# Kernel optimization log

Hardware: AMD Instinct MI355X
Metric: run time of the kernel (lower is better)

## Reference

```python
import jax, jax.numpy as jnp
import numpy as np

N_HEADS = 16
EMBED_DIM = 1024
HEAD_DIM = EMBED_DIM // N_HEADS  # 64
SRC_LEN = 64  # shifted-causal mask: key j visible iff j <= i + SRC_LEN
THETA = 10000.0


def _rope_tables(T, D, dtype):
    # angles[t, p] = t / theta^(2p/D), p in [0, D/2)
    freqs = 1.0 / (THETA ** (jnp.arange(0, D, 2, dtype=jnp.float32) / D))  # [D/2]
    ang = jnp.arange(T, dtype=jnp.float32)[:, None] * freqs[None, :]       # [T, D/2]
    return jnp.cos(ang).astype(dtype), jnp.sin(ang).astype(dtype)


def _apply_rope(x, cos, sin):
    # x: [B, T, H, D]; pairs along last dim act as complex numbers
    B, T, H, D = x.shape
    xp = x.reshape(B, T, H, D // 2, 2)
    x0, x1 = xp[..., 0], xp[..., 1]
    c = cos[None, :, None, :]  # [1, T, 1, D/2]
    s = sin[None, :, None, :]
    o0 = x0 * c - x1 * s
    o1 = x0 * s + x1 * c
    return jnp.stack([o0, o1], axis=-1).reshape(B, T, H, D)


def setup_inputs() -> dict:
    key = jax.random.key(0)
    ks = jax.random.split(key, 9)
    B, T, C = 2, 2048, EMBED_DIM
    sc = 1.0 / np.sqrt(C)
    inp = {
        "x_1": jax.random.normal(ks[0], (B, T, C), dtype=jnp.float32),
        "x_2": jax.random.normal(ks[1], (B, T, C), dtype=jnp.float32),
        "wq": jax.random.normal(ks[2], (C, C), dtype=jnp.float32) * sc,
        "bq": jax.random.normal(ks[3], (C,), dtype=jnp.float32) * sc,
        "wk": jax.random.normal(ks[4], (C, C), dtype=jnp.float32) * sc,
        "bk": jax.random.normal(ks[5], (C,), dtype=jnp.float32) * sc,
        "wv": jax.random.normal(ks[6], (C, C), dtype=jnp.float32) * sc,
        "bv": jax.random.normal(ks[7], (C,), dtype=jnp.float32) * sc,
        "wp": jax.random.normal(ks[8], (C, C), dtype=jnp.float32) * sc,
    }
    return inp


def reference(x_1, x_2, wq, bq, wk, bk, wv, bv, wp):
    B, T, C = x_1.shape
    H, D = N_HEADS, HEAD_DIM
    q = (x_1 @ wq.T + bq).reshape(B, T, H, D)
    k = (x_2 @ wk.T + bk).reshape(B, T, H, D)
    v = (x_2 @ wv.T + bv).reshape(B, T, H, D)
    cos, sin = _rope_tables(T, D, x_1.dtype)
    q = _apply_rope(q, cos, sin)
    k = _apply_rope(k, cos, sin)
    # attention with shifted causal mask
    attn = jnp.einsum("bihd,bjhd->bhij", q, k) * (D ** -0.5)
    i = jnp.arange(T)
    mask = i[None, :] <= i[:, None] + SRC_LEN  # [T, T], True = visible
    attn = jnp.where(mask[None, None, :, :], attn, -jnp.inf)
    attn = jax.nn.softmax(attn, axis=-1)
    out = jnp.einsum("bhij,bjhd->bihd", attn, v).reshape(B, T, C)
    return out @ wp.T
```

## Files before the change

kernel.cpp:

```cpp
#include <hip/hip_runtime.h>
#include <hip/hip_bf16.h>

typedef __bf16 v8bf __attribute__((ext_vector_type(8)));
typedef float  v4f  __attribute__((ext_vector_type(4)));

#define T_LEN 2048
#define NH 16
#define HD 64
#define BH 32
#define C_DIM 1024
#define SCQ 0.1803368801111737f

#define WS_X1B  ((size_t)0)
#define WS_X2B  ((size_t)8  << 20)
#define WS_W    ((size_t)16 << 20)
#define WS_CTAB ((size_t)24 << 20)
#define WS_STAB (WS_CTAB + 262144)
#define WS_Q    ((size_t)25 << 20)
#define WS_K    ((size_t)33 << 20)
#define WS_VT   ((size_t)41 << 20)
#define WS_O    ((size_t)0)

__device__ __forceinline__ unsigned short f2bf(float f) {
  unsigned int u = __float_as_uint(f);
  u += 0x7fffu + ((u >> 16) & 1u);
  return (unsigned short)(u >> 16);
}
__device__ __forceinline__ float bf2f(unsigned short h) {
  return __uint_as_float(((unsigned int)h) << 16);
}

__device__ __forceinline__ float xg_sum(float m) {
  m = m + __shfl_xor(m, 16, 64);
  m = m + __shfl_xor(m, 32, 64);
  return m;
}
__device__ __forceinline__ unsigned int packbf2hw(float lo, float hi) {
  unsigned short a = __builtin_bit_cast(unsigned short, (__bf16)lo);
  unsigned short b = __builtin_bit_cast(unsigned short, (__bf16)hi);
  return (unsigned int)a | ((unsigned int)b << 16);
}

__global__ __launch_bounds__(256) void cvt_kernel(
    const float* __restrict__ x1, const float* __restrict__ x2,
    const float* __restrict__ wq, const float* __restrict__ wk,
    const float* __restrict__ wv, const float* __restrict__ wp,
    unsigned short* __restrict__ x1b, unsigned short* __restrict__ x2b,
    unsigned short* __restrict__ wqb) {
  int i = blockIdx.x * 256 + threadIdx.x;
  if (i >= 3145728) return;
  const float* s; unsigned short* d; int off;
  if (i < 1048576) { s = x1; d = x1b; off = i; }
  else if (i < 2097152) { s = x2; d = x2b; off = i - 1048576; }
  else {
    int j = i - 2097152;
    int w = j >> 18;
    off = j & 262143;
    s = (w == 0) ? wq : (w == 1) ? wk : (w == 2) ? wv : wp;
    d = wqb + ((size_t)w * 1048576);
  }
  float4 v = ((const float4*)s)[off];
  ushort4 o;
  o.x = f2bf(v.x); o.y = f2bf(v.y); o.z = f2bf(v.z); o.w = f2bf(v.w);
  ((ushort4*)d)[off] = o;
}

__global__ __launch_bounds__(256) void tab_kernel(float* __restrict__ ctab,
                                                  float* __restrict__ stab) {
  int i = blockIdx.x * 256 + threadIdx.x;
  int t = i >> 5, f = i & 31;
  float freq = powf(10000.0f, -(float)f * (1.0f / 32.0f));
  float a = (float)t * freq;
  ctab[i] = cosf(a);
  stab[i] = sinf(a);
}

__global__ __launch_bounds__(256) void qk_gemm(
    const unsigned short* __restrict__ x1b, const unsigned short* __restrict__ x2b,
    const unsigned short* __restrict__ wall,
    const float* __restrict__ bq, const float* __restrict__ bk,
    const float* __restrict__ ctab, const float* __restrict__ stab,
    unsigned short* __restrict__ Qd, unsigned short* __restrict__ Kd) {
  int z = blockIdx.z;
  const unsigned short* A = (z == 0) ? x1b : x2b;
  const unsigned short* W = wall + (size_t)z * 1048576;
  const float* bias = (z == 0) ? bq : bk;
  unsigned short* dst = (z == 0) ? Qd : Kd;
  float scale = (z == 0) ? SCQ : 1.0f;

  __shared__ unsigned short lds[2][8192];
  int tid = threadIdx.x;
  int wave = tid >> 6, lane = tid & 63;
  int wm = wave >> 1, wn = wave & 1;
  int r = lane & 15, g = lane >> 4;
  int phys = blockIdx.y * (int)gridDim.x + blockIdx.x;
  int logical = (phys & 7) * 32 + (phys >> 3);
  int m0 = (logical >> 3) * 128, n0 = (logical & 7) * 128;
  int s3 = r & 3;

  v4f zero = {0.f, 0.f, 0.f, 0.f};
  v4f acc[4][4];
#pragma unroll
  for (int i = 0; i < 4; ++i)
#pragma unroll
    for (int j = 0; j < 4; ++j) acc[i][j] = zero;

  auto stage = [&](int b, int k0) {
    const unsigned short* Ab = A + (size_t)m0 * 1024 + k0;
    const unsigned short* Bb = W + (size_t)n0 * 1024 + k0;
#pragma unroll
    for (int it = 0; it < 2; ++it) {
      int c = it * 256 + tid;
      int row = c >> 2;
      int sc = (c & 3) ^ (row & 3);
      __builtin_amdgcn_global_load_lds(
          (const __attribute__((address_space(1))) void*)(Ab + (size_t)row * 1024 + sc * 8),
          (__attribute__((address_space(3))) void*)(&lds[b][0] + it * 2048 + wave * 512),
          16, 0, 0);
      __builtin_amdgcn_global_load_lds(
          (const __attribute__((address_space(1))) void*)(Bb + (size_t)row * 1024 + sc * 8),
          (__attribute__((address_space(3))) void*)(&lds[b][4096] + it * 2048 + wave * 512),
          16, 0, 0);
    }
  };

  stage(0, 0);
  asm volatile("s_waitcnt vmcnt(0)");
  __syncthreads();
  int cur = 0;

  for (int k0 = 0; k0 < 1024; k0 += 32) {
    if (k0 + 32 < 1024) stage(cur ^ 1, k0 + 32);
    v8bf af[4], bfr[4];
#pragma unroll
    for (int mf = 0; mf < 4; ++mf)
      af[mf] = *(const v8bf*)(&lds[cur][0] + (wm * 64 + mf * 16 + r) * 32 + ((g ^ s3) << 3));
#pragma unroll
    for (int nf = 0; nf < 4; ++nf)
      bfr[nf] = *(const v8bf*)(&lds[cur][4096] + (wn * 64 + nf * 16 + r) * 32 + ((g ^ s3) << 3));
#pragma unroll
    for (int mf = 0; mf < 4; ++mf)
#pragma unroll
      for (int nf = 0; nf < 4; ++nf)
        acc[mf][nf] = __builtin_amdgcn_mfma_f32_16x16x32_bf16(bfr[nf], af[mf], acc[mf][nf], 0, 0, 0);
    asm volatile("s_waitcnt vmcnt(0)");
    __syncthreads();
    cur ^= 1;
  }

#pragma unroll
  for (int mf = 0; mf < 4; ++mf) {
    int t = m0 + wm * 64 + mf * 16 + r;
    int b = t >> 11, tt = t & 2047;
#pragma unroll
    for (int nf = 0; nf < 4; ++nf) {
      int c0 = n0 + wn * 64 + nf * 16 + g * 4;
      int h = c0 >> 6, dh = c0 & 63;
      float4 b4 = *(const float4*)(bias + c0);
      int f0 = (dh >> 1);
      float2 cp = *(const float2*)(ctab + tt * 32 + f0);
      float2 sp = *(const float2*)(stab + tt * 32 + f0);
      float x0 = acc[mf][nf][0] + b4.x, x1 = acc[mf][nf][1] + b4.y;
      float x2 = acc[mf][nf][2] + b4.z, x3 = acc[mf][nf][3] + b4.w;
      ushort4 pk;
      pk.x = f2bf((x0 * cp.x - x1 * sp.x) * scale);
      pk.y = f2bf((x0 * sp.x + x1 * cp.x) * scale);
      pk.z = f2bf((x2 * cp.y - x3 * sp.y) * scale);
      pk.w = f2bf((x2 * sp.y + x3 * cp.y) * scale);
      *(ushort4*)(dst + (((size_t)(b * NH + h)) * T_LEN + tt) * HD + dh) = pk;
    }
  }
}

__global__ __launch_bounds__(256) void v_gemm(
    const unsigned short* __restrict__ x2b, const unsigned short* __restrict__ wv,
    const float* __restrict__ bv, unsigned short* __restrict__ VTd) {
  __shared__ unsigned short lds[2][8192];
  int tid = threadIdx.x;
  int wave = tid >> 6, lane = tid & 63;
  int wm = wave >> 1, wn = wave & 1;
  int r = lane & 15, g = lane >> 4;
  int phys = blockIdx.y * (int)gridDim.x + blockIdx.x;
  int logical = (phys & 7) * 32 + (phys >> 3);
  int m0 = (logical >> 3) * 128, n0 = (logical & 7) * 128;
  int s3 = r & 3;

  v4f zero = {0.f, 0.f, 0.f, 0.f};
  v4f acc[4][4];
#pragma unroll
  for (int i = 0; i < 4; ++i)
#pragma unroll
    for (int j = 0; j < 4; ++j) acc[i][j] = zero;

  auto stage = [&](int b, int k0) {
    const unsigned short* Ab = x2b + (size_t)m0 * 1024 + k0;
    const unsigned short* Bb = wv + (size_t)n0 * 1024 + k0;
#pragma unroll
    for (int it = 0; it < 2; ++it) {
      int c = it * 256 + tid;
      int row = c >> 2;
      int sc = (c & 3) ^ (row & 3);
      __builtin_amdgcn_global_load_lds(
          (const __attribute__((address_space(1))) void*)(Ab + (size_t)row * 1024 + sc * 8),
          (__attribute__((address_space(3))) void*)(&lds[b][0] + it * 2048 + wave * 512),
          16, 0, 0);
      __builtin_amdgcn_global_load_lds(
          (const __attribute__((address_space(1))) void*)(Bb + (size_t)row * 1024 + sc * 8),
          (__attribute__((address_space(3))) void*)(&lds[b][4096] + it * 2048 + wave * 512),
          16, 0, 0);
    }
  };

  stage(0, 0);
  asm volatile("s_waitcnt vmcnt(0)");
  __syncthreads();
  int cur = 0;

  for (int k0 = 0; k0 < 1024; k0 += 32) {
    if (k0 + 32 < 1024) stage(cur ^ 1, k0 + 32);
    v8bf af[4], bfr[4];
#pragma unroll
    for (int mf = 0; mf < 4; ++mf)
      af[mf] = *(const v8bf*)(&lds[cur][0] + (wm * 64 + mf * 16 + r) * 32 + ((g ^ s3) << 3));
#pragma unroll
    for (int nf = 0; nf < 4; ++nf)
      bfr[nf] = *(const v8bf*)(&lds[cur][4096] + (wn * 64 + nf * 16 + r) * 32 + ((g ^ s3) << 3));
#pragma unroll
    for (int mf = 0; mf < 4; ++mf)
#pragma unroll
      for (int nf = 0; nf < 4; ++nf)
        acc[mf][nf] = __builtin_amdgcn_mfma_f32_16x16x32_bf16(af[mf], bfr[nf], acc[mf][nf], 0, 0, 0);
    asm volatile("s_waitcnt vmcnt(0)");
    __syncthreads();
    cur ^= 1;
  }
#pragma unroll
  for (int nf = 0; nf < 4; ++nf) {
    int col = n0 + wn * 64 + nf * 16 + r;
    float bv_ = bv[col];
    int h = col >> 6, d = col & 63;
#pragma unroll
    for (int mf = 0; mf < 4; ++mf) {
      int row0 = m0 + wm * 64 + mf * 16 + g * 4;
      int b = row0 >> 11, t0 = row0 & 2047;
      ushort4 pk;
      pk.x = f2bf(acc[mf][nf][0] + bv_);
      pk.y = f2bf(acc[mf][nf][1] + bv_);
      pk.z = f2bf(acc[mf][nf][2] + bv_);
      pk.w = f2bf(acc[mf][nf][3] + bv_);
      *(ushort4*)(VTd + (((size_t)(b * NH + h)) * HD + d) * T_LEN + t0) = pk;
    }
  }
}

__global__ __launch_bounds__(256, 2) void attn_kernel(
    const unsigned short* __restrict__ Qd, const unsigned short* __restrict__ Kd,
    const unsigned short* __restrict__ VTd, unsigned short* __restrict__ Od) {
  int bh = blockIdx.x;
  int qt = (int)gridDim.y - 1 - (int)blockIdx.y;
  int tid = threadIdx.x, wave = tid >> 6, lane = tid & 63;
  int r = lane & 15, g = lane >> 4;
  int qmin = qt * 64 + wave * 16;
  const unsigned short* Qp = Qd + (size_t)bh * T_LEN * HD;
  const unsigned short* Kp = Kd + (size_t)bh * T_LEN * HD;
  const unsigned short* Vp = VTd + (size_t)bh * HD * T_LEN;

  __shared__ unsigned short kv[2][2][4096];
  __shared__ unsigned short plds[4][1024];

  v8bf qf0 = *(const v8bf*)(Qp + (size_t)(qmin + r) * HD + g * 8);
  v8bf qf1 = *(const v8bf*)(Qp + (size_t)(qmin + r) * HD + 32 + g * 8);

  v4f zero = {0.f, 0.f, 0.f, 0.f};
  v4f minus8 = {-8.f, -8.f, -8.f, -8.f};
  v4f oacc[4];
#pragma unroll
  for (int dt = 0; dt < 4; ++dt) oacc[dt] = zero;
  float li = 0.f;

  int ktiles = qt + 2; if (ktiles > 32) ktiles = 32;

  auto stage = [&](int b, int kt) {
    int j0 = kt * 64;
    const unsigned short* Kt = Kp + (size_t)j0 * HD;
#pragma unroll
    for (int is = 0; is < 2; ++is) {
      int q = is * 256 + tid;
      int row = q >> 3, c = q & 7;
      int swc = (c ^ (row & 7)) << 3;
      __builtin_amdgcn_global_load_lds(
          (const __attribute__((address_space(1))) void*)(Kt + row * 64 + swc),
          (__attribute__((address_space(3))) void*)(&kv[b][0][0] + is * 2048 + wave * 512),
          16, 0, 0);
      __builtin_amdgcn_global_load_lds(
          (const __attribute__((address_space(1))) void*)(Vp + (size_t)row * T_LEN + j0 + swc),
          (__attribute__((address_space(3))) void*)(&kv[b][1][0] + is * 2048 + wave * 512),
          16, 0, 0);
    }
  };

  stage(0, 0);
  asm volatile("s_waitcnt vmcnt(0)");
  __syncthreads();
  int cur = 0;

  unsigned short* plw = &plds[wave][0];
  int s7 = r & 7;
  int s8 = s7 << 3;

  for (int kt = 0; kt < ktiles; ++kt) {
    if (kt + 1 < ktiles) stage(cur ^ 1, kt + 1);
    int j0 = kt * 64;
    const unsigned short* kb = &kv[cur][0][0];
    const unsigned short* vb = &kv[cur][1][0];
    v8bf kf0[4], kf1[4], vf0[4], vf1[4];
#pragma unroll
    for (int nt = 0; nt < 4; ++nt) {
      int row = (nt * 16 + r) * 64;
      kf0[nt] = *(const v8bf*)(kb + row + ((g ^ s7) << 3));
      kf1[nt] = *(const v8bf*)(kb + row + (((4 + g) ^ s7) << 3));
      vf0[nt] = *(const v8bf*)(vb + row + ((g ^ s7) << 3));
      vf1[nt] = *(const v8bf*)(vb + row + (((4 + g) ^ s7) << 3));
    }
    v4f s[4];
#pragma unroll
    for (int nt = 0; nt < 4; ++nt) {
      v4f a = minus8;
      a = __builtin_amdgcn_mfma_f32_16x16x32_bf16(kf0[nt], qf0, a, 0, 0, 0);
      a = __builtin_amdgcn_mfma_f32_16x16x32_bf16(kf1[nt], qf1, a, 0, 0, 0);
      s[nt] = a;
    }
    if (j0 + 63 > qmin + 64) {
      int qi64 = qmin + r + 64;
#pragma unroll
      for (int nt = 0; nt < 4; ++nt)
#pragma unroll
        for (int rg = 0; rg < 4; ++rg) {
          int kj = j0 + nt * 16 + g * 4 + rg;
          if (kj > qi64) s[nt][rg] = -1e30f;
        }
    }
    float rs = 0.f;
#pragma unroll
    for (int nt = 0; nt < 4; ++nt)
#pragma unroll
      for (int rg = 0; rg < 4; ++rg) {
        float p = exp2f(s[nt][rg]);
        s[nt][rg] = p;
        rs += p;
      }
    li += rs;
#pragma unroll
    for (int nt = 0; nt < 4; ++nt) {
      uint2 w2;
      w2.x = packbf2hw(s[nt][0], s[nt][1]);
      w2.y = packbf2hw(s[nt][2], s[nt][3]);
      *(uint2*)(plw + r * 64 + (((nt << 4) + (g << 2)) ^ s8)) = w2;
    }
    v8bf pb0 = *(const v8bf*)(plw + r * 64 + ((g ^ s7) << 3));
    v8bf pb1 = *(const v8bf*)(plw + r * 64 + (((4 + g) ^ s7) << 3));
#pragma unroll
    for (int dt = 0; dt < 4; ++dt) {
      oacc[dt] = __builtin_amdgcn_mfma_f32_16x16x32_bf16(vf0[dt], pb0, oacc[dt], 0, 0, 0);
      oacc[dt] = __builtin_amdgcn_mfma_f32_16x16x32_bf16(vf1[dt], pb1, oacc[dt], 0, 0, 0);
    }
    asm volatile("s_waitcnt vmcnt(0)");
    __syncthreads();
    cur ^= 1;
  }
  float rli = 1.0f / xg_sum(li);
#pragma unroll
  for (int dt = 0; dt < 4; ++dt) {
    ushort4 pk;
    pk.x = __builtin_bit_cast(unsigned short, (__bf16)(oacc[dt][0] * rli));
    pk.y = __builtin_bit_cast(unsigned short, (__bf16)(oacc[dt][1] * rli));
    pk.z = __builtin_bit_cast(unsigned short, (__bf16)(oacc[dt][2] * rli));
    pk.w = __builtin_bit_cast(unsigned short, (__bf16)(oacc[dt][3] * rli));
    *(ushort4*)(Od + ((size_t)bh * T_LEN + qmin + r) * HD + dt * 16 + g * 4) = pk;
  }
}

__global__ __launch_bounds__(256) void proj_gemm(
    const unsigned short* __restrict__ Ob, const unsigned short* __restrict__ Wpb,
    float* __restrict__ out) {
  __shared__ unsigned short lds[2][8192];
  int tid = threadIdx.x;
  int wave = tid >> 6, lane = tid & 63;
  int wm = wave >> 1, wn = wave & 1;
  int r = lane & 15, g = lane >> 4;
  int phys = blockIdx.y * (int)gridDim.x + blockIdx.x;
  int logical = (phys & 7) * 32 + (phys >> 3);
  int m0 = (logical >> 3) * 128, n0 = (logical & 7) * 128;
  int s3 = r & 3;

  v4f zero = {0.f, 0.f, 0.f, 0.f};
  v4f acc[4][4];
#pragma unroll
  for (int i = 0; i < 4; ++i)
#pragma unroll
    for (int j = 0; j < 4; ++j) acc[i][j] = zero;

  auto stage = [&](int b, int k0) {
    int h = k0 >> 6;
#pragma unroll
    for (int it = 0; it < 2; ++it) {
      int c = it * 256 + tid;
      int row = c >> 2;
      int sc = (c & 3) ^ (row & 3);
      int k = k0 + sc * 8;
      int d = k & 63;
      int mrow = m0 + row;
      int bb = mrow >> 11, t = mrow & 2047;
      __builtin_amdgcn_global_load_lds(
          (const __attribute__((address_space(1))) void*)(Ob + (((size_t)(bb * NH + h)) * T_LEN + t) * HD + d),
          (__attribute__((address_space(3))) void*)(&lds[b][0] + it * 2048 + wave * 512),
          16, 0, 0);
      __builtin_amdgcn_global_load_lds(
          (const __attribute__((address_space(1))) void*)(Wpb + (size_t)(n0 + row) * 1024 + k),
          (__attribute__((address_space(3))) void*)(&lds[b][4096] + it * 2048 + wave * 512),
          16, 0, 0);
    }
  };

  stage(0, 0);
  asm volatile("s_waitcnt vmcnt(0)");
  __syncthreads();
  int cur = 0;

  for (int k0 = 0; k0 < 1024; k0 += 32) {
    if (k0 + 32 < 1024) stage(cur ^ 1, k0 + 32);
    v8bf af[4], bfr[4];
#pragma unroll
    for (int mf = 0; mf < 4; ++mf)
      af[mf] = *(const v8bf*)(&lds[cur][0] + (wm * 64 + mf * 16 + r) * 32 + ((g ^ s3) << 3));
#pragma unroll
    for (int nf = 0; nf < 4; ++nf)
      bfr[nf] = *(const v8bf*)(&lds[cur][4096] + (wn * 64 + nf * 16 + r) * 32 + ((g ^ s3) << 3));
#pragma unroll
    for (int mf = 0; mf < 4; ++mf)
#pragma unroll
      for (int nf = 0; nf < 4; ++nf)
        acc[mf][nf] = __builtin_amdgcn_mfma_f32_16x16x32_bf16(af[mf], bfr[nf], acc[mf][nf], 0, 0, 0);
    asm volatile("s_waitcnt vmcnt(0)");
    __syncthreads();
    cur ^= 1;
  }
#pragma unroll
  for (int mf = 0; mf < 4; ++mf)
#pragma unroll
    for (int nf = 0; nf < 4; ++nf) {
      int col = n0 + wn * 64 + nf * 16 + r;
      int row0 = m0 + wm * 64 + mf * 16 + g * 4;
#pragma unroll
      for (int rg = 0; rg < 4; ++rg)
        out[(size_t)(row0 + rg) * 1024 + col] = acc[mf][nf][rg];
    }
}

extern "C" void kernel_launch(void* const* d_in, const int* in_sizes, int n_in,
                              void* d_out, int out_size, void* d_ws, size_t ws_size,
                              hipStream_t stream) {
  const float* x1 = (const float*)d_in[0];
  const float* x2 = (const float*)d_in[1];
  const float* wq = (const float*)d_in[2];
  const float* bq = (const float*)d_in[3];
  const float* wk = (const float*)d_in[4];
  const float* bk = (const float*)d_in[5];
  const float* wv = (const float*)d_in[6];
  const float* bv = (const float*)d_in[7];
  const float* wp = (const float*)d_in[8];
  float* out = (float*)d_out;
  char* ws = (char*)d_ws;

  unsigned short* x1b = (unsigned short*)(ws + WS_X1B);
  unsigned short* x2b = (unsigned short*)(ws + WS_X2B);
  unsigned short* wqb = (unsigned short*)(ws + WS_W);
  unsigned short* wvb = wqb + 2 * 1048576;
  unsigned short* wpb = wqb + 3 * 1048576;
  float* ctab = (float*)(ws + WS_CTAB);
  float* stab = (float*)(ws + WS_STAB);
  unsigned short* Qd = (unsigned short*)(ws + WS_Q);
  unsigned short* Kd = (unsigned short*)(ws + WS_K);
  unsigned short* VTd = (unsigned short*)(ws + WS_VT);
  unsigned short* Od = (unsigned short*)(ws + WS_O);

  cvt_kernel<<<12288, 256, 0, stream>>>(x1, x2, wq, wk, wv, wp, x1b, x2b, wqb);
  tab_kernel<<<256, 256, 0, stream>>>(ctab, stab);
  qk_gemm<<<dim3(8, 32, 2), 256, 0, stream>>>(x1b, x2b, wqb, bq, bk, ctab, stab, Qd, Kd);
  v_gemm<<<dim3(8, 32), 256, 0, stream>>>(x2b, wvb, bv, VTd);
  attn_kernel<<<dim3(32, 32), 256, 0, stream>>>(Qd, Kd, VTd, Od);
  proj_gemm<<<dim3(8, 32), 256, 0, stream>>>(Od, wpb, out);
}
```

Before: 130.9 us.

## Load K and V fragments directly from global memory in attention kernel

Removes the double-buffered LDS staging of K and V tiles (global_load_lds plus block-wide barriers). Each wave now reads its MFMA fragments straight from global memory, with the V loads placed after the QK MFMAs. The launch-bounds occupancy hint is also relaxed. This drops LDS traffic and per-iteration syncs, but the four waves of a block now read the same K/V data redundantly through the cache, and load latency is exposed without prefetching.

```diff
diff --git a/kernel.cpp b/kernel.cpp
--- a/kernel.cpp
+++ b/kernel.cpp
@@ -253,7 +253,7 @@
   }
 }
 
-__global__ __launch_bounds__(256, 2) void attn_kernel(
+__global__ __launch_bounds__(256) void attn_kernel(
     const unsigned short* __restrict__ Qd, const unsigned short* __restrict__ Kd,
     const unsigned short* __restrict__ VTd, unsigned short* __restrict__ Od) {
   int bh = blockIdx.x;
@@ -265,7 +265,6 @@
   const unsigned short* Kp = Kd + (size_t)bh * T_LEN * HD;
   const unsigned short* Vp = VTd + (size_t)bh * HD * T_LEN;
 
-  __shared__ unsigned short kv[2][2][4096];
   __shared__ unsigned short plds[4][1024];
 
   v8bf qf0 = *(const v8bf*)(Qp + (size_t)(qmin + r) * HD + g * 8);
@@ -280,47 +279,18 @@
 
   int ktiles = qt + 2; if (ktiles > 32) ktiles = 32;
 
-  auto stage = [&](int b, int kt) {
-    int j0 = kt * 64;
-    const unsigned short* Kt = Kp + (size_t)j0 * HD;
-#pragma unroll
-    for (int is = 0; is < 2; ++is) {
-      int q = is * 256 + tid;
-      int row = q >> 3, c = q & 7;
-      int swc = (c ^ (row & 7)) << 3;
-      __builtin_amdgcn_global_load_lds(
-          (const __attribute__((address_space(1))) void*)(Kt + row * 64 + swc),
-          (__attribute__((address_space(3))) void*)(&kv[b][0][0] + is * 2048 + wave * 512),
-          16, 0, 0);
-      __builtin_amdgcn_global_load_lds(
-          (const __attribute__((address_space(1))) void*)(Vp + (size_t)row * T_LEN + j0 + swc),
-          (__attribute__((address_space(3))) void*)(&kv[b][1][0] + is * 2048 + wave * 512),
-          16, 0, 0);
-    }
-  };
-
-  stage(0, 0);
-  asm volatile("s_waitcnt vmcnt(0)");
-  __syncthreads();
-  int cur = 0;
-
   unsigned short* plw = &plds[wave][0];
   int s7 = r & 7;
   int s8 = s7 << 3;
 
   for (int kt = 0; kt < ktiles; ++kt) {
-    if (kt + 1 < ktiles) stage(cur ^ 1, kt + 1);
     int j0 = kt * 64;
-    const unsigned short* kb = &kv[cur][0][0];
-    const unsigned short* vb = &kv[cur][1][0];
-    v8bf kf0[4], kf1[4], vf0[4], vf1[4];
+    v8bf kf0[4], kf1[4];
 #pragma unroll
     for (int nt = 0; nt < 4; ++nt) {
-      int row = (nt * 16 + r) * 64;
-      kf0[nt] = *(const v8bf*)(kb + row + ((g ^ s7) << 3));
-      kf1[nt] = *(const v8bf*)(kb + row + (((4 + g) ^ s7) << 3));
-      vf0[nt] = *(const v8bf*)(vb + row + ((g ^ s7) << 3));
-      vf1[nt] = *(const v8bf*)(vb + row + (((4 + g) ^ s7) << 3));
+      const unsigned short* kr = Kp + (size_t)(j0 + nt * 16 + r) * HD;
+      kf0[nt] = *(const v8bf*)(kr + g * 8);
+      kf1[nt] = *(const v8bf*)(kr + 32 + g * 8);
     }
     v4f s[4];
 #pragma unroll
@@ -329,6 +299,13 @@
       a = __builtin_amdgcn_mfma_f32_16x16x32_bf16(kf0[nt], qf0, a, 0, 0, 0);
       a = __builtin_amdgcn_mfma_f32_16x16x32_bf16(kf1[nt], qf1, a, 0, 0, 0);
       s[nt] = a;
+    }
+    v8bf vf0[4], vf1[4];
+#pragma unroll
+    for (int nt = 0; nt < 4; ++nt) {
+      const unsigned short* vr = Vp + (size_t)(nt * 16 + r) * T_LEN + j0;
+      vf0[nt] = *(const v8bf*)(vr + g * 8);
+      vf1[nt] = *(const v8bf*)(vr + 32 + g * 8);
     }
     if (j0 + 63 > qmin + 64) {
       int qi64 = qmin + r + 64;
@@ -364,9 +341,6 @@
       oacc[dt] = __builtin_amdgcn_mfma_f32_16x16x32_bf16(vf0[dt], pb0, oacc[dt], 0, 0, 0);
       oacc[dt] = __builtin_amdgcn_mfma_f32_16x16x32_bf16(vf1[dt], pb1, oacc[dt], 0, 0, 0);
     }
-    asm volatile("s_waitcnt vmcnt(0)");
-    __syncthreads();
-    cur ^= 1;
   }
   float rli = 1.0f / xg_sum(li);
 #pragma unroll
```

Measured after the change: 228.5 us. +74.5%, slower.
